# Performance work log

Measured on AMD Instinct MI355X. Metric: run time of the kernel, lower is better.

Reference implementation:

```python
import math
import jax, jax.numpy as jnp
import numpy as np

D, H, NB, L, K = 45, 256, 6, 2, 8          # features, hidden, maf blocks, made hidden layers, spline bins
M = 3 * K - 1                               # params per feature (tails='linear')
TAIL = -math.log(1e-6)                      # tail_bound = -log(alpha)
MIN_BW = MIN_BH = MIN_D = 1e-3


def _masks():
    # nflows MADE sequential degrees (random_mask=False)
    d_in = np.arange(1, D + 1)
    d_h = (np.arange(H) % (D - 1)) + 1
    m0 = (d_h[:, None] >= d_in[None, :]).astype(np.float32)   # [H, D]
    mh = (d_h[:, None] >= d_h[None, :]).astype(np.float32)    # [H, H]
    d_out = np.repeat(d_in, M)                                 # nflows tile(): each degree repeated M times
    mf = (d_out[:, None] > d_h[None, :]).astype(np.float32)   # [D*M, H], strict for output layer
    return jnp.asarray(m0), jnp.asarray(mh), jnp.asarray(mf)


def _rq_spline(x, params):
    # x: [B, D]; params: [B, D, M]. unconstrained_rational_quadratic_spline, tails='linear'.
    uw = params[..., :K] / math.sqrt(H)        # nflows divides by sqrt(hidden_features)
    uh = params[..., K:2 * K] / math.sqrt(H)
    const = math.log(math.exp(1.0 - MIN_D) - 1.0)
    ud = jnp.pad(params[..., 2 * K:], ((0, 0), (0, 0), (1, 1)), constant_values=const)  # [B,D,K+1]
    inside = (x >= -TAIL) & (x <= TAIL)
    xc = jnp.clip(x, -TAIL, TAIL)

    def bin_edges(u, mn):
        p = jax.nn.softmax(u, -1)
        p = mn + (1.0 - mn * K) * p
        c = jnp.pad(jnp.cumsum(p, -1), ((0, 0), (0, 0), (1, 0)))
        c = 2.0 * TAIL * c - TAIL
        c = c.at[..., 0].set(-TAIL).at[..., -1].set(TAIL)
        return c, c[..., 1:] - c[..., :-1]

    cw, w = bin_edges(uw, MIN_BW)              # cumwidths [B,D,K+1], widths [B,D,K]
    ch, h = bin_edges(uh, MIN_BH)
    d = MIN_D + jax.nn.softplus(ud)            # derivatives [B,D,K+1]

    idx = jnp.clip(jnp.sum((xc[..., None] >= cw), -1) - 1, 0, K - 1)[..., None]
    g = lambda a: jnp.take_along_axis(a, idx, -1)[..., 0]
    icw, ibw, ich, ih = g(cw[..., :-1]), g(w), g(ch[..., :-1]), g(h)
    idelta = g(h / w)
    id0, id1 = g(d[..., :-1]), g(d[..., 1:])

    th = (xc - icw) / ibw
    th1 = th * (1.0 - th)
    den = idelta + (id0 + id1 - 2.0 * idelta) * th1
    y = ich + ih * (idelta * th * th + id0 * th1) / den
    lad = jnp.log(idelta * idelta * (id1 * th * th + 2.0 * idelta * th1 + id0 * (1.0 - th) ** 2)) - 2.0 * jnp.log(den)
    return jnp.where(inside, y, x), jnp.where(inside, lad, 0.0)


def setup_inputs() -> dict:
    key = jax.random.key(0)
    ks = jax.random.split(key, 10)
    B, s = 32768, 0.02
    return {
        "x": jax.random.normal(ks[0], (B, D), jnp.float32),
        "cond": jax.random.normal(ks[1], (B, 1), jnp.float32),
        "W0": jax.random.normal(ks[2], (NB, H, D), jnp.float32) * s,
        "b0": jax.random.normal(ks[3], (NB, H), jnp.float32) * s,
        "Wc": jax.random.normal(ks[4], (NB, H, 1), jnp.float32) * s,
        "bc": jax.random.normal(ks[5], (NB, H), jnp.float32) * s,
        "Wh": jax.random.normal(ks[6], (NB, L, H, H), jnp.float32) * s,
        "bh": jax.random.normal(ks[7], (NB, L, H), jnp.float32) * s,
        "Wf": jax.random.normal(ks[8], (NB, D * M, H), jnp.float32) * s,
        "bf": jax.random.normal(ks[9], (NB, D * M), jnp.float32) * s,
    }


def reference(x, cond, W0, b0, Wc, bc, Wh, bh, Wf, bf):
    m0, mh, mf = _masks()
    z = x
    ld = jnp.zeros(x.shape[0], x.dtype)
    for b in range(NB):  # CompositeTransform of NB MAF blocks
        hid = z @ (W0[b] * m0).T + b0[b] + cond @ Wc[b].T + bc[b]
        for l in range(L):  # MaskedFeedforwardBlock: linear -> ReLU (dropout=0, no BN)
            hid = jax.nn.relu(hid @ (Wh[b, l] * mh).T + bh[b, l])
        params = (hid @ (Wf[b] * mf).T + bf[b]).reshape(z.shape[0], D, M)
        z, lad = _rq_spline(z, params)
        ld = ld + lad.sum(-1)
    log_z = 0.5 * D * math.log(2.0 * math.pi)
    return -0.5 * jnp.sum(z * z, axis=1) - log_z + ld
```

## Files before the change

### kernel.cpp

```cpp
#include <hip/hip_runtime.h>


typedef __bf16 bf16;
typedef __bf16 bf16x8 __attribute__((ext_vector_type(8)));
typedef float  f32x16 __attribute__((ext_vector_type(16)));

#define TAILF  13.815510557964274f
#define LOGZ   41.352233994210265f

#define WS_W0M   0
#define WS_WHM   196608
#define WS_WFM   1769472
#define WS_BEFF  5210112
#define WS_BFP   5216256
#define WS_WCC   5243136
#define WS_BHP   5249280
#define WS_NEED  5261568

#define N_W0  (6*256*64)
#define N_WH  (6*2*256*256)
#define N_WF  (6*5*224*256)
#define N_PREP (N_W0 + N_WH + N_WF)

__device__ __forceinline__ int s_deg(int s) {
    return (s < 216) ? (s / 6) : (36 + (s - 216) / 5);
}
__device__ __forceinline__ int s_orig(int s) {
    int d, rk;
    if (s < 216) { d = s / 6; rk = s - d * 6; }
    else { int u = s - 216; d = 36 + u / 5; rk = u - (u / 5) * 5; }
    return d + 44 * rk;
}

__global__ void prep_all(const float* __restrict__ W0, const float* __restrict__ b0,
                         const float* __restrict__ Wc, const float* __restrict__ bc,
                         const float* __restrict__ Wh, const float* __restrict__ Wf,
                         const float* __restrict__ bfv, const float* __restrict__ bh,
                         bf16* __restrict__ W0m, bf16* __restrict__ Whm,
                         bf16* __restrict__ Wfm,
                         float* __restrict__ beff, float* __restrict__ bfp,
                         float* __restrict__ Wcc, float* __restrict__ bhp)
{
    int idx = blockIdx.x * 256 + threadIdx.x;
    if (idx < N_W0) {
        int j = idx & 7, lane = (idx >> 3) & 63, chunk = idx >> 9;
        int kt = chunk & 3, cg = (chunk >> 2) & 7, b = chunk >> 5;
        int col = cg * 32 + (lane & 31);
        int k   = kt * 16 + (lane >> 5) * 8 + j;
        int o   = s_orig(col);
        float v = 0.f;
        if (k < 45 && s_deg(col) >= k)
            v = W0[(b * 256 + o) * 45 + k];
        W0m[idx] = (bf16)v;
        if (k == 0) {
            beff[b * 256 + col] = b0[b * 256 + o] + bc[b * 256 + o];
            Wcc[b * 256 + col]  = Wc[b * 256 + o];
        }
    } else if (idx < N_W0 + N_WH) {
        int id = idx - N_W0;
        int j = id & 7, lane = (id >> 3) & 63, chunk = id >> 9;
        int kt = chunk & 15, cg = (chunk >> 4) & 7, bl = chunk >> 7;
        int col = cg * 32 + (lane & 31);
        int k   = kt * 16 + (lane >> 5) * 8 + j;
        int oc  = s_orig(col), ok = s_orig(k);
        float v = (s_deg(col) >= s_deg(k)) ? Wh[bl * 65536 + oc * 256 + ok] : 0.f;
        Whm[id] = (bf16)v;
        if (k == 0)
            bhp[bl * 256 + col] = bh[bl * 256 + oc];
    } else if (idx < N_PREP) {
        int id = idx - (N_W0 + N_WH);
        int j = id & 7, lane = (id >> 3) & 63, chunk = id >> 9;
        int kt = chunk & 15, t2 = chunk >> 4;
        int cg = t2 % 7, bg = t2 / 7;
        int b  = bg / 5, g = bg - 5 * b;
        int col = cg * 32 + (lane & 31);
        int k   = kt * 16 + (lane >> 5) * 8 + j;
        int ok  = s_orig(k);
        int f   = 9 * g + col / 23;
        int m   = col - (col / 23) * 23;
        bool valid = (col < 207);
        float v = 0.f;
        if (valid && (f > s_deg(k)))
            v = Wf[(b * 1035 + f * 23 + m) * 256 + ok];
        Wfm[id] = (bf16)v;
        if (k == 0)
            bfp[bg * 224 + col] = valid ? bfv[b * 1035 + f * 23 + m] : 0.f;
    }
}

#define SO_ZF    0
#define SO_ZB    11776
#define SO_HIDA  18944
#define SO_PBUF  52736
#define SO_COND  80528
#define SO_LD    80784
#define SMEM_BYTES 81040

#define PBF 1544

__constant__ unsigned char IN_NP[8]     = {1,1,1,1,1,1,2,2};
__constant__ unsigned char HID_NP[8]    = {2,3,3,5,6,6,8,8};
__constant__ unsigned char OUT_NP[5][7] = {
    {1,1,1,1,2,2,2},
    {2,3,3,3,3,4,4},
    {4,4,5,5,5,5,5},
    {6,6,6,6,7,7,7},
    {7,8,8,8,8,8,8}};

__device__ __forceinline__ void do_spline9(int fb, float* zf, bf16* zb,
                                           const bf16* pbuf, int t, float& lad_acc);

template<int MODE>
__device__ __forceinline__ void epi32(const f32x16& acc, int cg, int hf,
    const float* __restrict__ bias, const float* __restrict__ wcol,
    const float* condl, bf16* dst, int l31, int kh8)
{
    const int col = cg * 32 + l31;
    if (MODE == 2 && col >= 207) return;
    const float bv = bias[col];
    const int rb = (kh8 >> 1) + hf * 32;
    if (MODE == 2) {
        const int fl = col / 23, m = col - fl * 23;
        bf16* dp = dst + fl * PBF + m;
        #pragma unroll
        for (int r = 0; r < 16; ++r) {
            int row = (r & 3) + 8 * (r >> 2) + rb;
            dp[row * 24] = (bf16)(acc[r] + bv);
        }
    } else {
        const float wcv = (MODE == 0) ? wcol[col] : 0.f;
        #pragma unroll
        for (int r = 0; r < 16; ++r) {
            int row = (r & 3) + 8 * (r >> 2) + rb;
            float v = acc[r] + bv;
            if (MODE == 0) v += condl[row] * wcv;
            if (MODE == 1) v = fmaxf(v, 0.f);
            dst[row * 264 + col] = (bf16)v;
        }
    }
}

template<int KTFULL, int MODE, bool SPLINE>
__device__ __forceinline__ void gemm64(
    const bf16* Asrc, const int lda,
    const bf16* __restrict__ Wp,
    const float* __restrict__ bias, const float* __restrict__ wcol,
    const float* condl, bf16* dst,
    int cg, int np, int halfmask,
    int lane, bool preEpiSync,
    int fb, float* zf, bf16* zb, const bf16* pbuf, int t, float* lad_acc)
{
    const int l31 = lane & 31;
    const int kh8 = (lane >> 5) * 8;
    const bf16* Bp  = Wp + (size_t)cg * (KTFULL * 512) + lane * 8;
    const bf16* Alo = Asrc + l31 * lda + kh8;
    const bf16* Ahi = Alo + 32 * lda;

    f32x16 acc0 = {}, acc1 = {};
    bf16x8 rA0, rA1, rB0, rB1;

#define LB(c)  (*reinterpret_cast<const bf16x8*>(Bp + (size_t)(c) * 512))
#define LAL(c) (*reinterpret_cast<const bf16x8*>(Alo + (c) * 16))
#define LAH(c) (*reinterpret_cast<const bf16x8*>(Ahi + (c) * 16))
#define CHUNK(breg, c) { \
    bf16x8 a0_ = LAL(c), a1_ = LAH(c); \
    acc0 = __builtin_amdgcn_mfma_f32_32x32x16_bf16(a0_, breg, acc0, 0, 0, 0); \
    acc1 = __builtin_amdgcn_mfma_f32_32x32x16_bf16(a1_, breg, acc1, 0, 0, 0); }
#define LP(r0, r1, p) { r0 = LB(2*(p)); r1 = LB(2*(p)+1); }
#define CP(r0, r1, p) { CHUNK(r0, 2*(p)) CHUNK(r1, 2*(p)+1) }

    LP(rA0, rA1, 0);
    if (np > 1) LP(rB0, rB1, 1);

    if constexpr (SPLINE)
        do_spline9(fb, zf, zb, pbuf, t, *lad_acc);

    int p = 0;
    #pragma unroll 1
    while (p + 2 < np) {
        CP(rA0, rA1, p);
        LP(rA0, rA1, p + 2);
        CP(rB0, rB1, p + 1);
        if (p + 3 < np) LP(rB0, rB1, p + 3);
        p += 2;
    }
    CP(rA0, rA1, p);
    if (np - p > 1) CP(rB0, rB1, p + 1);

#undef LB
#undef LAL
#undef LAH
#undef CHUNK
#undef LP
#undef CP

    if (preEpiSync) __syncthreads();

    if (halfmask & 1) epi32<MODE>(acc0, cg, 0, bias, wcol, condl, dst, l31, kh8);
    if (halfmask & 2) epi32<MODE>(acc1, cg, 1, bias, wcol, condl, dst, l31, kh8);
    __syncthreads();
}

__device__ __forceinline__ void do_spline9(int fb, float* zf, bf16* zb,
                                           const bf16* pbuf, int t, float& lad_acc)
{
    #pragma unroll 1
    for (int task = t; task < 576; task += 512) {
        int fl = task >> 6, r = task & 63;
        const bf16* pp = pbuf + fl * PBF + r * 24;
        bf16x8 q0 = *reinterpret_cast<const bf16x8*>(pp);
        bf16x8 q1 = *reinterpret_cast<const bf16x8*>(pp + 8);
        bf16x8 q2 = *reinterpret_cast<const bf16x8*>(pp + 16);
        float P[23];
        #pragma unroll
        for (int m = 0; m < 8; ++m) P[m]      = (float)q0[m];
        #pragma unroll
        for (int m = 0; m < 8; ++m) P[8 + m]  = (float)q1[m];
        #pragma unroll
        for (int m = 0; m < 7; ++m) P[16 + m] = (float)q2[m];

        float xin = zf[r * 46 + fb + fl];
        float xc  = fminf(fmaxf(xin, -TAILF), TAILF);
        bool inside = (xin >= -TAILF) && (xin <= TAILF);

        float mw = P[0];
        #pragma unroll
        for (int i = 1; i < 8; ++i) mw = fmaxf(mw, P[i]);
        float ew[8], sw = 0.f;
        #pragma unroll
        for (int i = 0; i < 8; ++i) { ew[i] = __expf((P[i] - mw) * 0.0625f); sw += ew[i]; }
        float rws = 0.992f / sw;
        float cw[9]; cw[0] = -TAILF;
        #pragma unroll
        for (int i = 0; i < 8; ++i)
            cw[i + 1] = cw[i] + 2.f * TAILF * (1e-3f + ew[i] * rws);
        cw[8] = TAILF;
        float wb[8];
        #pragma unroll
        for (int i = 0; i < 8; ++i) wb[i] = cw[i + 1] - cw[i];

        float mh = P[8];
        #pragma unroll
        for (int i = 1; i < 8; ++i) mh = fmaxf(mh, P[8 + i]);
        float eh[8], sh = 0.f;
        #pragma unroll
        for (int i = 0; i < 8; ++i) { eh[i] = __expf((P[8 + i] - mh) * 0.0625f); sh += eh[i]; }
        float rhs = 0.992f / sh;
        float ch[9]; ch[0] = -TAILF;
        #pragma unroll
        for (int i = 0; i < 8; ++i)
            ch[i + 1] = ch[i] + 2.f * TAILF * (1e-3f + eh[i] * rhs);
        ch[8] = TAILF;
        float hb[8];
        #pragma unroll
        for (int i = 0; i < 8; ++i) hb[i] = ch[i + 1] - ch[i];

        float dd[9];
        dd[0] = 1.0f; dd[8] = 1.0f;
        #pragma unroll
        for (int i = 1; i < 8; ++i)
            dd[i] = 1e-3f + __logf(1.f + __expf(P[15 + i]));

        float icw = cw[0], ich = ch[0], ibw = wb[0], ibh = hb[0];
        float id0 = dd[0], id1 = dd[1];
        #pragma unroll
        for (int i = 1; i < 8; ++i) {
            bool ge = xc >= cw[i];
            icw = ge ? cw[i] : icw;  ich = ge ? ch[i] : ich;
            ibw = ge ? wb[i] : ibw;  ibh = ge ? hb[i] : ibh;
            id0 = ge ? dd[i] : id0;  id1 = ge ? dd[i + 1] : id1;
        }

        float th  = (xc - icw) / ibw;
        float th1 = th * (1.f - th);
        float dl  = ibh / ibw;
        float den = dl + (id0 + id1 - 2.f * dl) * th1;
        float yy  = ich + ibh * (dl * th * th + id0 * th1) / den;
        float num = dl * dl * (id1 * th * th + 2.f * dl * th1
                               + id0 * (1.f - th) * (1.f - th));
        float lad = __logf(num) - 2.f * __logf(den);

        if (inside) {
            zf[r * 46 + fb + fl] = yy;
            zb[r * 56 + fb + fl] = (bf16)yy;
        }
        lad_acc += inside ? lad : 0.f;
    }
}

__global__ __launch_bounds__(512, 4) void maf_main(
    const float* __restrict__ x, const float* __restrict__ cond,
    const bf16* __restrict__ W0m, const bf16* __restrict__ Whm,
    const bf16* __restrict__ Wfm,
    const float* __restrict__ beff, const float* __restrict__ bfp,
    const float* __restrict__ Wcc, const float* __restrict__ bhp,
    float* __restrict__ out, int B)
{
    extern __shared__ char smem[];
    float* zf    = (float*)(smem + SO_ZF);
    bf16*  zb    = (bf16*)(smem + SO_ZB);
    bf16*  hidA  = (bf16*)(smem + SO_HIDA);
    bf16*  pbuf  = (bf16*)(smem + SO_PBUF);
    float* condl = (float*)(smem + SO_COND);
    float* ldl   = (float*)(smem + SO_LD);

    const int t    = threadIdx.x;
    const int r0   = blockIdx.x * 64;
    const int w    = t >> 6;
    const int lane = t & 63;
    const int wu   = __builtin_amdgcn_readfirstlane(w);

    for (int i = t; i < 64 * 11; i += 512) {
        int r = i / 11, c = i - (i / 11) * 11;
        zb[r * 56 + 45 + c] = (bf16)0.f;
    }
    if (t < 8) hidA[t] = (bf16)0.f;
    for (int i = t; i < 64 * 45; i += 512) {
        int r = i / 45, f = i - (i / 45) * 45;
        float v = (r0 + r < B) ? x[(size_t)(r0 + r) * 45 + f] : 0.f;
        zf[r * 46 + f] = v;
        zb[r * 56 + f] = (bf16)v;
    }
    if (t < 64) {
        condl[t] = (r0 + t < B) ? cond[r0 + t] : 0.f;
        ldl[t]   = 0.f;
    }
    __syncthreads();

    float lad_acc = 0.f;

    const int inNp  = IN_NP[wu];
    const int hidNp = HID_NP[wu];
    const int ocg   = (wu <= 5) ? wu : 6;
    const int ohm   = (wu <= 5) ? 3 : ((wu == 6) ? 1 : 2);

    #pragma unroll 1
    for (int b = 0; b < 6; ++b) {
        gemm64<4, 0, false>(zb, 56, W0m + b * 16384,
                            beff + b * 256, Wcc + b * 256, condl,
                            hidA, wu, inNp, 3, lane, false,
                            0, nullptr, nullptr, nullptr, 0, nullptr);
        #pragma unroll 1
        for (int l = 0; l < 2; ++l)
            gemm64<16, 1, false>(hidA, 264, Whm + (b * 2 + l) * 65536,
                                 bhp + (b * 2 + l) * 256, nullptr, condl,
                                 hidA, wu, hidNp, 3, lane, true,
                                 0, nullptr, nullptr, nullptr, 0, nullptr);
        gemm64<16, 2, false>(hidA, 264, Wfm + (size_t)(b * 5) * 57344,
                             bfp + (b * 5) * 224, nullptr, condl,
                             pbuf, ocg, OUT_NP[0][ocg], ohm, lane, false,
                             0, nullptr, nullptr, nullptr, 0, nullptr);
        #pragma unroll 1
        for (int g = 1; g < 5; ++g) {
            gemm64<16, 2, true>(hidA, 264, Wfm + (size_t)(b * 5 + g) * 57344,
                                bfp + (b * 5 + g) * 224, nullptr, condl,
                                pbuf, ocg, OUT_NP[g][ocg], ohm, lane, true,
                                (g - 1) * 9, zf, zb, pbuf, t, &lad_acc);
        }
        do_spline9(36, zf, zb, pbuf, t, lad_acc);
        __syncthreads();
    }

    atomicAdd(&ldl[t & 63], lad_acc);
    __syncthreads();

    if (t < 64 && r0 + t < B) {
        float s = 0.f;
        #pragma unroll
        for (int f = 0; f < 45; ++f) { float v = zf[t * 46 + f]; s += v * v; }
        out[r0 + t] = -0.5f * s - LOGZ + ldl[t];
    }
}

extern "C" void kernel_launch(void* const* d_in, const int* in_sizes, int n_in,
                              void* d_out, int out_size, void* d_ws, size_t ws_size,
                              hipStream_t stream)
{
    const float* x    = (const float*)d_in[0];
    const float* cond = (const float*)d_in[1];
    const float* W0   = (const float*)d_in[2];
    const float* b0   = (const float*)d_in[3];
    const float* Wc   = (const float*)d_in[4];
    const float* bc   = (const float*)d_in[5];
    const float* Wh   = (const float*)d_in[6];
    const float* bh   = (const float*)d_in[7];
    const float* Wf   = (const float*)d_in[8];
    const float* bfv  = (const float*)d_in[9];
    float* out = (float*)d_out;

    const int B = in_sizes[0] / 45;
    if (ws_size < (size_t)WS_NEED) return;

    char* ws = (char*)d_ws;
    bf16*  W0m  = (bf16*)(ws + WS_W0M);
    bf16*  Whm  = (bf16*)(ws + WS_WHM);
    bf16*  Wfm  = (bf16*)(ws + WS_WFM);
    float* beff = (float*)(ws + WS_BEFF);
    float* bfp  = (float*)(ws + WS_BFP);
    float* Wcc  = (float*)(ws + WS_WCC);
    float* bhp  = (float*)(ws + WS_BHP);

    prep_all<<<(N_PREP + 255) / 256, 256, 0, stream>>>(
        W0, b0, Wc, bc, Wh, Wf, bfv, bh, W0m, Whm, Wfm, beff, bfp, Wcc, bhp);

    (void)hipFuncSetAttribute((const void*)maf_main,
                              hipFuncAttributeMaxDynamicSharedMemorySize,
                              SMEM_BYTES);

    const int nwg = (B + 63) / 64;
    maf_main<<<nwg, 512, SMEM_BYTES, stream>>>(
        x, cond, W0m, Whm, Wfm, beff, bfp, Wcc, bhp, out, B);
}
```

Measured before the change: 320.8 us.

## Use 9 waves and run spline serially after each output GEMM group

The workgroup grows from 512 to 576 threads so that every spline task (9 features × 64 rows) gets its own thread, which removes the strided task loop. Spline evaluation is no longer interleaved inside the next output GEMM group's prefetch window. Each group's GEMM now runs, then its spline, then a barrier. The ninth wave takes no part in the GEMMs, and the launch bound hint changes from 4 to 8. This gives up the earlier overlap of spline math with GEMM loads, and the extra barrier per group may add synchronisation cost.

```diff
diff --git a/kernel.cpp b/kernel.cpp
--- a/kernel.cpp
+++ b/kernel.cpp
@@ -7,6 +7,7 @@
 
 #define TAILF  13.815510557964274f
 #define LOGZ   41.352233994210265f
+#define NT     576
 
 #define WS_W0M   0
 #define WS_WHM   196608
@@ -107,9 +108,6 @@
     {6,6,6,6,7,7,7},
     {7,8,8,8,8,8,8}};
 
-__device__ __forceinline__ void do_spline9(int fb, float* zf, bf16* zb,
-                                           const bf16* pbuf, int t, float& lad_acc);
-
 template<int MODE>
 __device__ __forceinline__ void epi32(const f32x16& acc, int cg, int hf,
     const float* __restrict__ bias, const float* __restrict__ wcol,
@@ -140,15 +138,14 @@
     }
 }
 
-template<int KTFULL, int MODE, bool SPLINE>
+template<int KTFULL, int MODE>
 __device__ __forceinline__ void gemm64(
     const bf16* Asrc, const int lda,
     const bf16* __restrict__ Wp,
     const float* __restrict__ bias, const float* __restrict__ wcol,
     const float* condl, bf16* dst,
     int cg, int np, int halfmask,
-    int lane, bool preEpiSync,
-    int fb, float* zf, bf16* zb, const bf16* pbuf, int t, float* lad_acc)
+    int lane, bool preEpiSync)
 {
     const int l31 = lane & 31;
     const int kh8 = (lane >> 5) * 8;
@@ -157,7 +154,6 @@
     const bf16* Ahi = Alo + 32 * lda;
 
     f32x16 acc0 = {}, acc1 = {};
-    bf16x8 rA0, rA1, rB0, rB1;
 
 #define LB(c)  (*reinterpret_cast<const bf16x8*>(Bp + (size_t)(c) * 512))
 #define LAL(c) (*reinterpret_cast<const bf16x8*>(Alo + (c) * 16))
@@ -169,23 +165,23 @@
 #define LP(r0, r1, p) { r0 = LB(2*(p)); r1 = LB(2*(p)+1); }
 #define CP(r0, r1, p) { CHUNK(r0, 2*(p)) CHUNK(r1, 2*(p)+1) }
 
-    LP(rA0, rA1, 0);
-    if (np > 1) LP(rB0, rB1, 1);
-
-    if constexpr (SPLINE)
-        do_spline9(fb, zf, zb, pbuf, t, *lad_acc);
-
-    int p = 0;
-    #pragma unroll 1
-    while (p + 2 < np) {
+    if (np > 0) {
+        bf16x8 rA0, rA1, rB0, rB1;
+        LP(rA0, rA1, 0);
+        if (np > 1) LP(rB0, rB1, 1);
+
+        int p = 0;
+        #pragma unroll 1
+        while (p + 2 < np) {
+            CP(rA0, rA1, p);
+            LP(rA0, rA1, p + 2);
+            CP(rB0, rB1, p + 1);
+            if (p + 3 < np) LP(rB0, rB1, p + 3);
+            p += 2;
+        }
         CP(rA0, rA1, p);
-        LP(rA0, rA1, p + 2);
-        CP(rB0, rB1, p + 1);
-        if (p + 3 < np) LP(rB0, rB1, p + 3);
-        p += 2;
-    }
-    CP(rA0, rA1, p);
-    if (np - p > 1) CP(rB0, rB1, p + 1);
+        if (np - p > 1) CP(rB0, rB1, p + 1);
+    }
 
 #undef LB
 #undef LAL
@@ -204,91 +200,88 @@
 __device__ __forceinline__ void do_spline9(int fb, float* zf, bf16* zb,
                                            const bf16* pbuf, int t, float& lad_acc)
 {
-    #pragma unroll 1
-    for (int task = t; task < 576; task += 512) {
-        int fl = task >> 6, r = task & 63;
-        const bf16* pp = pbuf + fl * PBF + r * 24;
-        bf16x8 q0 = *reinterpret_cast<const bf16x8*>(pp);
-        bf16x8 q1 = *reinterpret_cast<const bf16x8*>(pp + 8);
-        bf16x8 q2 = *reinterpret_cast<const bf16x8*>(pp + 16);
-        float P[23];
-        #pragma unroll
-        for (int m = 0; m < 8; ++m) P[m]      = (float)q0[m];
-        #pragma unroll
-        for (int m = 0; m < 8; ++m) P[8 + m]  = (float)q1[m];
-        #pragma unroll
-        for (int m = 0; m < 7; ++m) P[16 + m] = (float)q2[m];
-
-        float xin = zf[r * 46 + fb + fl];
-        float xc  = fminf(fmaxf(xin, -TAILF), TAILF);
-        bool inside = (xin >= -TAILF) && (xin <= TAILF);
-
-        float mw = P[0];
-        #pragma unroll
-        for (int i = 1; i < 8; ++i) mw = fmaxf(mw, P[i]);
-        float ew[8], sw = 0.f;
-        #pragma unroll
-        for (int i = 0; i < 8; ++i) { ew[i] = __expf((P[i] - mw) * 0.0625f); sw += ew[i]; }
-        float rws = 0.992f / sw;
-        float cw[9]; cw[0] = -TAILF;
-        #pragma unroll
-        for (int i = 0; i < 8; ++i)
-            cw[i + 1] = cw[i] + 2.f * TAILF * (1e-3f + ew[i] * rws);
-        cw[8] = TAILF;
-        float wb[8];
-        #pragma unroll
-        for (int i = 0; i < 8; ++i) wb[i] = cw[i + 1] - cw[i];
-
-        float mh = P[8];
-        #pragma unroll
-        for (int i = 1; i < 8; ++i) mh = fmaxf(mh, P[8 + i]);
-        float eh[8], sh = 0.f;
-        #pragma unroll
-        for (int i = 0; i < 8; ++i) { eh[i] = __expf((P[8 + i] - mh) * 0.0625f); sh += eh[i]; }
-        float rhs = 0.992f / sh;
-        float ch[9]; ch[0] = -TAILF;
-        #pragma unroll
-        for (int i = 0; i < 8; ++i)
-            ch[i + 1] = ch[i] + 2.f * TAILF * (1e-3f + eh[i] * rhs);
-        ch[8] = TAILF;
-        float hb[8];
-        #pragma unroll
-        for (int i = 0; i < 8; ++i) hb[i] = ch[i + 1] - ch[i];
-
-        float dd[9];
-        dd[0] = 1.0f; dd[8] = 1.0f;
-        #pragma unroll
-        for (int i = 1; i < 8; ++i)
-            dd[i] = 1e-3f + __logf(1.f + __expf(P[15 + i]));
-
-        float icw = cw[0], ich = ch[0], ibw = wb[0], ibh = hb[0];
-        float id0 = dd[0], id1 = dd[1];
-        #pragma unroll
-        for (int i = 1; i < 8; ++i) {
-            bool ge = xc >= cw[i];
-            icw = ge ? cw[i] : icw;  ich = ge ? ch[i] : ich;
-            ibw = ge ? wb[i] : ibw;  ibh = ge ? hb[i] : ibh;
-            id0 = ge ? dd[i] : id0;  id1 = ge ? dd[i + 1] : id1;
-        }
-
-        float th  = (xc - icw) / ibw;
-        float th1 = th * (1.f - th);
-        float dl  = ibh / ibw;
-        float den = dl + (id0 + id1 - 2.f * dl) * th1;
-        float yy  = ich + ibh * (dl * th * th + id0 * th1) / den;
-        float num = dl * dl * (id1 * th * th + 2.f * dl * th1
-                               + id0 * (1.f - th) * (1.f - th));
-        float lad = __logf(num) - 2.f * __logf(den);
-
-        if (inside) {
-            zf[r * 46 + fb + fl] = yy;
-            zb[r * 56 + fb + fl] = (bf16)yy;
-        }
-        lad_acc += inside ? lad : 0.f;
-    }
-}
-
-__global__ __launch_bounds__(512, 4) void maf_main(
+    const int fl = t >> 6, r = t & 63;
+    const bf16* pp = pbuf + fl * PBF + r * 24;
+    bf16x8 q0 = *reinterpret_cast<const bf16x8*>(pp);
+    bf16x8 q1 = *reinterpret_cast<const bf16x8*>(pp + 8);
+    bf16x8 q2 = *reinterpret_cast<const bf16x8*>(pp + 16);
+    float P[23];
+    #pragma unroll
+    for (int m = 0; m < 8; ++m) P[m]      = (float)q0[m];
+    #pragma unroll
+    for (int m = 0; m < 8; ++m) P[8 + m]  = (float)q1[m];
+    #pragma unroll
+    for (int m = 0; m < 7; ++m) P[16 + m] = (float)q2[m];
+
+    float xin = zf[r * 46 + fb + fl];
+    float xc  = fminf(fmaxf(xin, -TAILF), TAILF);
+    bool inside = (xin >= -TAILF) && (xin <= TAILF);
+
+    float mw = P[0];
+    #pragma unroll
+    for (int i = 1; i < 8; ++i) mw = fmaxf(mw, P[i]);
+    float ew[8], sw = 0.f;
+    #pragma unroll
+    for (int i = 0; i < 8; ++i) { ew[i] = __expf((P[i] - mw) * 0.0625f); sw += ew[i]; }
+    float rws = 0.992f / sw;
+    float cw[9]; cw[0] = -TAILF;
+    #pragma unroll
+    for (int i = 0; i < 8; ++i)
+        cw[i + 1] = cw[i] + 2.f * TAILF * (1e-3f + ew[i] * rws);
+    cw[8] = TAILF;
+    float wb[8];
+    #pragma unroll
+    for (int i = 0; i < 8; ++i) wb[i] = cw[i + 1] - cw[i];
+
+    float mh = P[8];
+    #pragma unroll
+    for (int i = 1; i < 8; ++i) mh = fmaxf(mh, P[8 + i]);
+    float eh[8], sh = 0.f;
+    #pragma unroll
+    for (int i = 0; i < 8; ++i) { eh[i] = __expf((P[8 + i] - mh) * 0.0625f); sh += eh[i]; }
+    float rhs = 0.992f / sh;
+    float ch[9]; ch[0] = -TAILF;
+    #pragma unroll
+    for (int i = 0; i < 8; ++i)
+        ch[i + 1] = ch[i] + 2.f * TAILF * (1e-3f + eh[i] * rhs);
+    ch[8] = TAILF;
+    float hb[8];
+    #pragma unroll
+    for (int i = 0; i < 8; ++i) hb[i] = ch[i + 1] - ch[i];
+
+    float dd[9];
+    dd[0] = 1.0f; dd[8] = 1.0f;
+    #pragma unroll
+    for (int i = 1; i < 8; ++i)
+        dd[i] = 1e-3f + __logf(1.f + __expf(P[15 + i]));
+
+    float icw = cw[0], ich = ch[0], ibw = wb[0], ibh = hb[0];
+    float id0 = dd[0], id1 = dd[1];
+    #pragma unroll
+    for (int i = 1; i < 8; ++i) {
+        bool ge = xc >= cw[i];
+        icw = ge ? cw[i] : icw;  ich = ge ? ch[i] : ich;
+        ibw = ge ? wb[i] : ibw;  ibh = ge ? hb[i] : ibh;
+        id0 = ge ? dd[i] : id0;  id1 = ge ? dd[i + 1] : id1;
+    }
+
+    float th  = (xc - icw) / ibw;
+    float th1 = th * (1.f - th);
+    float dl  = ibh / ibw;
+    float den = dl + (id0 + id1 - 2.f * dl) * th1;
+    float yy  = ich + ibh * (dl * th * th + id0 * th1) / den;
+    float num = dl * dl * (id1 * th * th + 2.f * dl * th1
+                           + id0 * (1.f - th) * (1.f - th));
+    float lad = __logf(num) - 2.f * __logf(den);
+
+    if (inside) {
+        zf[r * 46 + fb + fl] = yy;
+        zb[r * 56 + fb + fl] = (bf16)yy;
+    }
+    lad_acc += inside ? lad : 0.f;
+}
+
+__global__ __launch_bounds__(NT, 8) void maf_main(
     const float* __restrict__ x, const float* __restrict__ cond,
     const bf16* __restrict__ W0m, const bf16* __restrict__ Whm,
     const bf16* __restrict__ Wfm,
@@ -310,12 +303,12 @@
     const int lane = t & 63;
     const int wu   = __builtin_amdgcn_readfirstlane(w);
 
-    for (int i = t; i < 64 * 11; i += 512) {
+    for (int i = t; i < 64 * 11; i += NT) {
         int r = i / 11, c = i - (i / 11) * 11;
         zb[r * 56 + 45 + c] = (bf16)0.f;
     }
     if (t < 8) hidA[t] = (bf16)0.f;
-    for (int i = t; i < 64 * 45; i += 512) {
+    for (int i = t; i < 64 * 45; i += NT) {
         int r = i / 45, f = i - (i / 45) * 45;
         float v = (r0 + r < B) ? x[(size_t)(r0 + r) * 45 + f] : 0.f;
         zf[r * 46 + f] = v;
@@ -329,36 +322,34 @@
 
     float lad_acc = 0.f;
 
-    const int inNp  = IN_NP[wu];
-    const int hidNp = HID_NP[wu];
-    const int ocg   = (wu <= 5) ? wu : 6;
-    const int ohm   = (wu <= 5) ? 3 : ((wu == 6) ? 1 : 2);
+    const bool gw    = (wu < 8);
+    const int  inNp  = gw ? IN_NP[wu]  : 0;
+    const int  hidNp = gw ? HID_NP[wu] : 0;
+    const int  ghm   = gw ? 3 : 0;
+    int ocg, ohm;
+    if (wu <= 5)      { ocg = wu; ohm = 3; }
+    else if (wu == 6) { ocg = 6;  ohm = 1; }
+    else if (wu == 7) { ocg = 6;  ohm = 2; }
+    else              { ocg = 0;  ohm = 0; }
 
     #pragma unroll 1
     for (int b = 0; b < 6; ++b) {
-        gemm64<4, 0, false>(zb, 56, W0m + b * 16384,
-                            beff + b * 256, Wcc + b * 256, condl,
-                            hidA, wu, inNp, 3, lane, false,
-                            0, nullptr, nullptr, nullptr, 0, nullptr);
+        gemm64<4, 0>(zb, 56, W0m + b * 16384,
+                     beff + b * 256, Wcc + b * 256, condl,
+                     hidA, gw ? wu : 0, inNp, ghm, lane, false);
         #pragma unroll 1
         for (int l = 0; l < 2; ++l)
-            gemm64<16, 1, false>(hidA, 264, Whm + (b * 2 + l) * 65536,
-                                 bhp + (b * 2 + l) * 256, nullptr, condl,
-                                 hidA, wu, hidNp, 3, lane, true,
-                                 0, nullptr, nullptr, nullptr, 0, nullptr);
-        gemm64<16, 2, false>(hidA, 264, Wfm + (size_t)(b * 5) * 57344,
-                             bfp + (b * 5) * 224, nullptr, condl,
-                             pbuf, ocg, OUT_NP[0][ocg], ohm, lane, false,
-                             0, nullptr, nullptr, nullptr, 0, nullptr);
+            gemm64<16, 1>(hidA, 264, Whm + (b * 2 + l) * 65536,
+                          bhp + (b * 2 + l) * 256, nullptr, condl,
+                          hidA, gw ? wu : 0, hidNp, ghm, lane, true);
         #pragma unroll 1
-        for (int g = 1; g < 5; ++g) {
-            gemm64<16, 2, true>(hidA, 264, Wfm + (size_t)(b * 5 + g) * 57344,
-                                bfp + (b * 5 + g) * 224, nullptr, condl,
-                                pbuf, ocg, OUT_NP[g][ocg], ohm, lane, true,
-                                (g - 1) * 9, zf, zb, pbuf, t, &lad_acc);
+        for (int g = 0; g < 5; ++g) {
+            gemm64<16, 2>(hidA, 264, Wfm + (size_t)(b * 5 + g) * 57344,
+                          bfp + (b * 5 + g) * 224, nullptr, condl,
+                          pbuf, ocg, ohm ? OUT_NP[g][ocg] : 0, ohm, lane, false);
+            do_spline9(g * 9, zf, zb, pbuf, t, lad_acc);
+            __syncthreads();
         }
-        do_spline9(36, zf, zb, pbuf, t, lad_acc);
-        __syncthreads();
     }
 
     atomicAdd(&ldl[t & 63], lad_acc);
@@ -408,6 +399,6 @@
                               SMEM_BYTES);
 
     const int nwg = (B + 63) / 64;
-    maf_main<<<nwg, 512, SMEM_BYTES, stream>>>(
+    maf_main<<<nwg, NT, SMEM_BYTES, stream>>>(
         x, cond, W0m, Whm, Wfm, beff, bfp, Wcc, bhp, out, B);
 }
```

After: 386.0 us. 1.2x slower.
